# Kernel tuning notes

Hardware: AMD Instinct MI355X
Metric: run time of the kernel (lower is better)

Reference implementation:

```python
import jax, jax.numpy as jnp
import numpy as np

T_STEPS = 64   # number of actions (T-1 in the torch code)
BATCH = 512
STATE = 256
ACTION = 64
BELIEF = 1024
HIDDEN = 1024
EMB = 1024
MIN_STD = 0.1


def setup_inputs() -> dict:
    key = jax.random.key(0)
    ks = jax.random.split(key, 16)
    def w(k, shape):
        return jax.random.normal(k, shape, jnp.float32) * 0.02
    return {
        "s_0": jax.random.normal(ks[0], (BATCH, STATE), jnp.float32),
        "A": jax.random.normal(ks[1], (T_STEPS, BATCH, ACTION), jnp.float32),
        "b_0": jax.random.normal(ks[2], (BATCH, BELIEF), jnp.float32),
        "O": jax.random.normal(ks[3], (T_STEPS, BATCH, EMB), jnp.float32),
        "M": jnp.ones((T_STEPS, BATCH, 1), jnp.float32),
        "noise_pri": jax.random.normal(ks[4], (T_STEPS, BATCH, STATE), jnp.float32),
        "noise_pos": jax.random.normal(ks[5], (T_STEPS, BATCH, STATE), jnp.float32),
        # learned parameters (torch nn.Linear convention: y = x @ W.T + b)
        "W_sa": w(ks[6], (BELIEF, STATE + ACTION)), "b_sa": jnp.zeros((BELIEF,), jnp.float32),
        "W_ih": w(ks[7], (3 * BELIEF, BELIEF)), "b_ih": jnp.zeros((3 * BELIEF,), jnp.float32),
        "W_hh": w(ks[8], (3 * BELIEF, BELIEF)), "b_hh": jnp.zeros((3 * BELIEF,), jnp.float32),
        "W_bpri": w(ks[9], (HIDDEN, BELIEF)), "b_bpri": jnp.zeros((HIDDEN,), jnp.float32),
        "W_spri": w(ks[10], (2 * STATE, HIDDEN)), "b_spri": jnp.zeros((2 * STATE,), jnp.float32),
        "W_bpos": w(ks[11], (HIDDEN, BELIEF + EMB)), "b_bpos": jnp.zeros((HIDDEN,), jnp.float32),
        "W_spos": w(ks[12], (2 * STATE, HIDDEN)), "b_spos": jnp.zeros((2 * STATE,), jnp.float32),
    }


def reference(s_0, A, b_0, O, M, noise_pri, noise_pos,
              W_sa, b_sa, W_ih, b_ih, W_hh, b_hh,
              W_bpri, b_bpri, W_spri, b_spri,
              W_bpos, b_bpos, W_spos, b_spos):
    act = jax.nn.relu  # cfg.activation_function = 'relu'

    def gru_cell(x, h):
        # torch GRUCell gate order: r, z, n
        gi = x @ W_ih.T + b_ih      # [B, 3*BELIEF]
        gh = h @ W_hh.T + b_hh
        i_r, i_z, i_n = jnp.split(gi, 3, axis=1)
        h_r, h_z, h_n = jnp.split(gh, 3, axis=1)
        r = jax.nn.sigmoid(i_r + h_r)
        z = jax.nn.sigmoid(i_z + h_z)
        n = jnp.tanh(i_n + r * h_n)
        return (1.0 - z) * n + z * h

    def step(carry, xs):
        b, s = carry  # belief [B,BELIEF], posterior state [B,STATE]
        a_t, o_t, m_t, eps_p, eps_q = xs
        s_in = s * m_t  # non-terminal mask
        x = act(jnp.concatenate([s_in, a_t], axis=1) @ W_sa.T + b_sa)
        b_new = gru_cell(x, b)
        # prior
        pri = act(b_new @ W_bpri.T + b_bpri) @ W_spri.T + b_spri
        mu_p, hp = jnp.split(pri, 2, axis=1)
        std_p = jax.nn.softplus(hp) + MIN_STD
        s_p = mu_p + std_p * eps_p
        # posterior (uses current observation embedding)
        pos = act(jnp.concatenate([b_new, o_t], axis=1) @ W_bpos.T + b_bpos) @ W_spos.T + b_spos
        mu_q, hq = jnp.split(pos, 2, axis=1)
        std_q = jax.nn.softplus(hq) + MIN_STD
        s_q = mu_q + std_q * eps_q
        return (b_new, s_q), (b_new, s_p, mu_p, std_p, s_q, mu_q, std_q)

    (_, _), ys = jax.lax.scan(step, (b_0, s_0), (A, O, M, noise_pri, noise_pos))
    B_out, S_pri, MU_pri, STD_pri, S_pos, MU_pos, STD_pos = ys
    return B_out, S_pri, MU_pri, STD_pri, S_pos, MU_pos, STD_pos
```

## Files before the change

### kernel.cpp

```cpp
#include <hip/hip_runtime.h>
#include <hip/hip_bf16.h>
#include <math.h>

typedef short bf16x8 __attribute__((ext_vector_type(8)));
typedef float f32x4 __attribute__((ext_vector_type(4)));
typedef unsigned short u16;

#define NT 64
#define NB 512
#define NS 256
#define NA 64
#define NBEL 1024

#define OUT_B      0
#define OUT_SPRI   33554432
#define OUT_MUPRI  41943040
#define OUT_STDPRI 50331648
#define OUT_SPOS   58720256
#define OUT_MUPOS  67108864
#define OUT_STDPOS 75497472

__device__ __forceinline__ f32x4 mfma16(bf16x8 a, bf16x8 b, f32x4 c) {
  return __builtin_amdgcn_mfma_f32_16x16x32_bf16(a, b, c, 0, 0, 0);
}

__device__ __forceinline__ u16 f2bf(float f) {
  union { float f; unsigned u; } v; v.f = f;
  return (u16)((v.u + 0x7FFFu + ((v.u >> 16) & 1u)) >> 16);
}

__device__ __forceinline__ bf16x8 ld8bf(const u16* p) { return *(const bf16x8*)p; }

__device__ __forceinline__ bf16x8 cvt8(const float* p) {
  const float4 lo = *(const float4*)p;
  const float4 hi = *(const float4*)(p + 4);
  bf16x8 v;
  v[0] = (short)f2bf(lo.x); v[1] = (short)f2bf(lo.y);
  v[2] = (short)f2bf(lo.z); v[3] = (short)f2bf(lo.w);
  v[4] = (short)f2bf(hi.x); v[5] = (short)f2bf(hi.y);
  v[6] = (short)f2bf(hi.z); v[7] = (short)f2bf(hi.w);
  return v;
}

__device__ __forceinline__ float sigm(float x) { return 1.f / (1.f + __expf(-x)); }
__device__ __forceinline__ float softplus_(float x) {
  if (x > 20.f) return x;
  return log1pf(__expf(x));
}

#define ZACC(acc) { acc[0][0] = (f32x4){0.f,0.f,0.f,0.f}; acc[0][1] = (f32x4){0.f,0.f,0.f,0.f}; \
                    acc[1][0] = (f32x4){0.f,0.f,0.f,0.f}; acc[1][1] = (f32x4){0.f,0.f,0.f,0.f}; }

#define Q4(acc, a0v, a1v, b0v, b1v) \
  acc[0][0] = mfma16(a0v, b0v, acc[0][0]); \
  acc[0][1] = mfma16(a0v, b1v, acc[0][1]); \
  acc[1][0] = mfma16(a1v, b0v, acc[1][0]); \
  acc[1][1] = mfma16(a1v, b1v, acc[1][1]);

__device__ __forceinline__ void red_write(float* L, f32x4 (&acc)[2][2], int l) {
  const int base = l * 16;
#pragma unroll
  for (int i = 0; i < 2; ++i)
#pragma unroll
    for (int j = 0; j < 2; ++j)
#pragma unroll
      for (int q = 0; q < 4; ++q)
        L[base + (i * 2 + j) * 4 + q] = acc[i][j][q];
}
__device__ __forceinline__ void red_add(const float* L, f32x4 (&acc)[2][2], int l) {
  const int base = l * 16;
#pragma unroll
  for (int i = 0; i < 2; ++i)
#pragma unroll
    for (int j = 0; j < 2; ++j)
#pragma unroll
      for (int q = 0; q < 4; ++q)
        acc[i][j][q] += L[base + (i * 2 + j) * 4 + q];
}

__global__ __launch_bounds__(256) void cvt_weights_k(
    const float* __restrict__ wsa, const float* __restrict__ wih,
    const float* __restrict__ whh, const float* __restrict__ wbpri,
    const float* __restrict__ wspri, const float* __restrict__ wbpos,
    const float* __restrict__ wspos, u16* __restrict__ dst) {
  const int S0 = 327680;
  const int S1 = S0 + 3145728;
  const int S2 = S1 + 3145728;
  const int S3 = S2 + 1048576;
  const int S4 = S3 + 524288;
  const int S5 = S4 + 2097152;
  const int S6 = S5 + 524288;
  for (int i = blockIdx.x * blockDim.x + threadIdx.x; i < S6;
       i += gridDim.x * blockDim.x) {
    float v;
    if (i < S0) v = wsa[i];
    else if (i < S1) v = wih[i - S0];
    else if (i < S2) v = whh[i - S1];
    else if (i < S3) v = wbpri[i - S2];
    else if (i < S4) v = wspri[i - S3];
    else if (i < S5) v = wbpos[i - S4];
    else v = wspos[i - S5];
    dst[i] = f2bf(v);
  }
}

__global__ __launch_bounds__(256) void init_carry_k(
    const float* __restrict__ s0, const float* __restrict__ b0,
    const float* __restrict__ Mptr, u16* __restrict__ smask,
    u16* __restrict__ bbf0, float* __restrict__ hf) {
  for (int i = blockIdx.x * blockDim.x + threadIdx.x; i < NB * NBEL;
       i += gridDim.x * blockDim.x) {
    float b = b0[i];
    bbf0[i] = f2bf(b);
    hf[i] = b;
    if (i < NB * NS) {
      int row = i >> 8;
      smask[i] = f2bf(s0[i] * Mptr[row]);
    }
  }
}

__global__ __launch_bounds__(512, 2) void kA(
    const u16* __restrict__ smask, const float* __restrict__ Af,
    const u16* __restrict__ wsa, const float* __restrict__ bsa,
    u16* __restrict__ xbf, const float* __restrict__ Of,
    const u16* __restrict__ wbpos, float* __restrict__ hbO, int t) {
  __shared__ float lred[4][1024];
  const int l = threadIdx.x & 63, r16 = l & 15, kq = l >> 4;
  const int wid8 = threadIdx.x >> 6;
  const int wid = wid8 & 3, kh = wid8 >> 2;
  if (blockIdx.x < 128) {
    const int g = blockIdx.x, bm = g >> 4, bn = g & 15;
    const int row0 = bm * 64 + (wid >> 1) * 32;
    const int col0 = bn * 64 + (wid & 1) * 32;
    f32x4 acc[2][2]; ZACC(acc);
    const u16* A0 = smask + (row0 + r16) * NS + kq * 8;
    const u16* A1 = A0 + 16 * NS;
    const u16* B0 = wsa + (size_t)(col0 + r16) * 320 + kq * 8;
    const u16* B1 = B0 + 16 * 320;
    if (kh == 0) {
#pragma unroll
      for (int k = 0; k < 160; k += 32) {
        bf16x8 a0 = ld8bf(A0 + k), a1 = ld8bf(A1 + k);
        bf16x8 b0 = ld8bf(B0 + k), b1 = ld8bf(B1 + k);
        Q4(acc, a0, a1, b0, b1);
      }
    } else {
#pragma unroll
      for (int k = 160; k < 256; k += 32) {
        bf16x8 a0 = ld8bf(A0 + k), a1 = ld8bf(A1 + k);
        bf16x8 b0 = ld8bf(B0 + k), b1 = ld8bf(B1 + k);
        Q4(acc, a0, a1, b0, b1);
      }
      const float* F0 = Af + (size_t)t * (NB * NA) + (row0 + r16) * NA + kq * 8;
      const float* F1 = F0 + 16 * NA;
      const u16* C0 = wsa + (size_t)(col0 + r16) * 320 + 256 + kq * 8;
      const u16* C1 = C0 + 16 * 320;
#pragma unroll
      for (int k = 0; k < 64; k += 32) {
        bf16x8 a0 = cvt8(F0 + k), a1 = cvt8(F1 + k);
        bf16x8 b0 = ld8bf(C0 + k), b1 = ld8bf(C1 + k);
        Q4(acc, a0, a1, b0, b1);
      }
      red_write(lred[wid], acc, l);
    }
    __syncthreads();
    if (kh == 0) {
      red_add(lred[wid], acc, l);
#pragma unroll
      for (int i = 0; i < 2; ++i)
#pragma unroll
        for (int j = 0; j < 2; ++j)
#pragma unroll
          for (int q = 0; q < 4; ++q) {
            const int row = row0 + i * 16 + kq * 4 + q;
            const int col = col0 + j * 16 + r16;
            xbf[row * NBEL + col] = f2bf(fmaxf(acc[i][j][q] + bsa[col], 0.f));
          }
    }
  } else {
    const int g = blockIdx.x - 128, bm = g >> 4, bn = g & 15;
    const int row0 = bm * 64 + (wid >> 1) * 32;
    const int col0 = bn * 64 + (wid & 1) * 32;
    f32x4 acc[2][2]; ZACC(acc);
    const float* F0 = Of + (size_t)t * (NB * NBEL) + (row0 + r16) * NBEL + kh * 512 + kq * 8;
    const float* F1 = F0 + 16 * NBEL;
    const u16* B0 = wbpos + (size_t)(col0 + r16) * 2048 + 1024 + kh * 512 + kq * 8;
    const u16* B1 = B0 + 16 * 2048;
#pragma unroll 4
    for (int k = 0; k < 512; k += 32) {
      bf16x8 a0 = cvt8(F0 + k), a1 = cvt8(F1 + k);
      bf16x8 b0 = ld8bf(B0 + k), b1 = ld8bf(B1 + k);
      Q4(acc, a0, a1, b0, b1);
    }
    if (kh == 1) red_write(lred[wid], acc, l);
    __syncthreads();
    if (kh == 0) {
      red_add(lred[wid], acc, l);
#pragma unroll
      for (int i = 0; i < 2; ++i)
#pragma unroll
        for (int j = 0; j < 2; ++j)
#pragma unroll
          for (int q = 0; q < 4; ++q) {
            const int row = row0 + i * 16 + kq * 4 + q;
            const int col = col0 + j * 16 + r16;
            hbO[row * NBEL + col] = acc[i][j][q];
          }
    }
  }
}

__global__ __launch_bounds__(512, 2) void kB(
    const u16* __restrict__ xbf, const u16* __restrict__ bprev,
    const u16* __restrict__ wih, const u16* __restrict__ whh,
    const float* __restrict__ bih, const float* __restrict__ bhh,
    float* __restrict__ hf, u16* __restrict__ bcur, float* __restrict__ out,
    const u16* __restrict__ wbpri, const float* __restrict__ bbpri,
    u16* __restrict__ hpri, int t) {
  __shared__ float lred[4][3][1024];
  const int l = threadIdx.x & 63, r16 = l & 15, kq = l >> 4;
  const int wid8 = threadIdx.x >> 6;
  const int wid = wid8 & 3, kh = wid8 >> 2;
  if (blockIdx.x < 128) {
    if (t >= NT) return;
    const int g = blockIdx.x, bm = g >> 4, bn = g & 15;
    const int row0 = bm * 64 + (wid >> 1) * 32;
    const int col0 = bn * 64 + (wid & 1) * 32;
    f32x4 ar[2][2], az[2][2], an[2][2];
    ZACC(ar); ZACC(az); ZACC(an);
    const u16* Asrc = (kh == 0) ? xbf : bprev;
    const u16* W = (kh == 0) ? wih : whh;
    const u16* A0 = Asrc + (row0 + r16) * NBEL + kq * 8;
    const u16* A1 = A0 + 16 * NBEL;
    const u16* Br0 = W + (size_t)(col0 + r16) * NBEL + kq * 8;
    const u16* Br1 = Br0 + 16 * NBEL;
    const u16* Bz0 = W + (size_t)(col0 + 1024 + r16) * NBEL + kq * 8;
    const u16* Bz1 = Bz0 + 16 * NBEL;
    const u16* Bn0 = W + (size_t)(col0 + 2048 + r16) * NBEL + kq * 8;
    const u16* Bn1 = Bn0 + 16 * NBEL;
#pragma unroll 4
    for (int k = 0; k < NBEL; k += 32) {
      bf16x8 a0 = ld8bf(A0 + k), a1 = ld8bf(A1 + k);
      bf16x8 b0 = ld8bf(Br0 + k), b1 = ld8bf(Br1 + k);
      Q4(ar, a0, a1, b0, b1);
      bf16x8 c0 = ld8bf(Bz0 + k), c1 = ld8bf(Bz1 + k);
      Q4(az, a0, a1, c0, c1);
      bf16x8 d0 = ld8bf(Bn0 + k), d1 = ld8bf(Bn1 + k);
      Q4(an, a0, a1, d0, d1);
    }
    if (kh == 1) {
      red_write(lred[wid][0], ar, l);
      red_write(lred[wid][1], az, l);
      red_write(lred[wid][2], an, l);
    }
    __syncthreads();
    if (kh == 0) {
      const int base = l * 16;
#pragma unroll
      for (int i = 0; i < 2; ++i)
#pragma unroll
        for (int j = 0; j < 2; ++j)
#pragma unroll
          for (int q = 0; q < 4; ++q) {
            const int row = row0 + i * 16 + kq * 4 + q;
            const int c = col0 + j * 16 + r16;
            const int li = base + (i * 2 + j) * 4 + q;
            const float r = sigm(ar[i][j][q] + bih[c] + lred[wid][0][li] + bhh[c]);
            const float z = sigm(az[i][j][q] + bih[c + 1024] + lred[wid][1][li] + bhh[c + 1024]);
            const float n = tanhf(an[i][j][q] + bih[c + 2048] +
                                  r * (lred[wid][2][li] + bhh[c + 2048]));
            const float h = hf[row * NBEL + c];
            const float bnew = (1.f - z) * n + z * h;
            hf[row * NBEL + c] = bnew;
            bcur[row * NBEL + c] = f2bf(bnew);
            out[OUT_B + (size_t)t * (NB * NBEL) + row * NBEL + c] = bnew;
          }
    }
  } else {
    if (t < 1) return;
    const int g = blockIdx.x - 128, bm = g >> 4, bn = g & 15;
    const int row0 = bm * 64 + (wid >> 1) * 32;
    const int col0 = bn * 64 + (wid & 1) * 32;
    f32x4 acc[2][2]; ZACC(acc);
    const u16* A0 = bprev + (row0 + r16) * NBEL + kh * 512 + kq * 8;
    const u16* A1 = A0 + 16 * NBEL;
    const u16* B0 = wbpri + (size_t)(col0 + r16) * NBEL + kh * 512 + kq * 8;
    const u16* B1 = B0 + 16 * NBEL;
#pragma unroll 4
    for (int k = 0; k < 512; k += 32) {
      bf16x8 a0 = ld8bf(A0 + k), a1 = ld8bf(A1 + k);
      bf16x8 b0 = ld8bf(B0 + k), b1 = ld8bf(B1 + k);
      Q4(acc, a0, a1, b0, b1);
    }
    if (kh == 1) red_write(lred[wid][0], acc, l);
    __syncthreads();
    if (kh == 0) {
      red_add(lred[wid][0], acc, l);
#pragma unroll
      for (int i = 0; i < 2; ++i)
#pragma unroll
        for (int j = 0; j < 2; ++j)
#pragma unroll
          for (int q = 0; q < 4; ++q) {
            const int row = row0 + i * 16 + kq * 4 + q;
            const int col = col0 + j * 16 + r16;
            hpri[row * NBEL + col] = f2bf(fmaxf(acc[i][j][q] + bbpri[col], 0.f));
          }
    }
  }
}

__global__ __launch_bounds__(512, 2) void kC(
    const u16* __restrict__ bcur, const u16* __restrict__ wbpos,
    const float* __restrict__ bbpos, const float* __restrict__ hbO,
    u16* __restrict__ hbbf,
    const u16* __restrict__ hpri, const u16* __restrict__ wspri,
    const float* __restrict__ bspri, const float* __restrict__ npri,
    float* __restrict__ out, int t) {
  __shared__ float lred[4][2][1024];
  const int l = threadIdx.x & 63, r16 = l & 15, kq = l >> 4;
  const int wid8 = threadIdx.x >> 6;
  const int wid = wid8 & 3, kh = wid8 >> 2;
  if (blockIdx.x < 128) {
    if (t >= NT) return;
    const int g = blockIdx.x, bm = g >> 4, bn = g & 15;
    const int row0 = bm * 64 + (wid >> 1) * 32;
    const int col0 = bn * 64 + (wid & 1) * 32;
    f32x4 acc[2][2]; ZACC(acc);
    const u16* A0 = bcur + (row0 + r16) * NBEL + kh * 512 + kq * 8;
    const u16* A1 = A0 + 16 * NBEL;
    const u16* B0 = wbpos + (size_t)(col0 + r16) * 2048 + kh * 512 + kq * 8;
    const u16* B1 = B0 + 16 * 2048;
#pragma unroll 4
    for (int k = 0; k < 512; k += 32) {
      bf16x8 a0 = ld8bf(A0 + k), a1 = ld8bf(A1 + k);
      bf16x8 b0 = ld8bf(B0 + k), b1 = ld8bf(B1 + k);
      Q4(acc, a0, a1, b0, b1);
    }
    if (kh == 1) red_write(lred[wid][0], acc, l);
    __syncthreads();
    if (kh == 0) {
      red_add(lred[wid][0], acc, l);
#pragma unroll
      for (int i = 0; i < 2; ++i)
#pragma unroll
        for (int j = 0; j < 2; ++j)
#pragma unroll
          for (int q = 0; q < 4; ++q) {
            const int row = row0 + i * 16 + kq * 4 + q;
            const int col = col0 + j * 16 + r16;
            const float v = acc[i][j][q] + hbO[row * NBEL + col] + bbpos[col];
            hbbf[row * NBEL + col] = f2bf(fmaxf(v, 0.f));
          }
    }
  } else {
    if (t < 1) return;
    const int g = blockIdx.x - 128, bm = g >> 2, bn = g & 3;
    const int row0 = bm * 64 + (wid >> 1) * 32;
    const int c0 = bn * 64 + (wid & 1) * 32;
    f32x4 am[2][2], ah[2][2];
    ZACC(am); ZACC(ah);
    const u16* A0 = hpri + (row0 + r16) * NBEL + kh * 512 + kq * 8;
    const u16* A1 = A0 + 16 * NBEL;
    const u16* Bm0 = wspri + (size_t)(c0 + r16) * NBEL + kh * 512 + kq * 8;
    const u16* Bm1 = Bm0 + 16 * NBEL;
    const u16* Bh0 = wspri + (size_t)(c0 + 256 + r16) * NBEL + kh * 512 + kq * 8;
    const u16* Bh1 = Bh0 + 16 * NBEL;
#pragma unroll 4
    for (int k = 0; k < 512; k += 32) {
      bf16x8 a0 = ld8bf(A0 + k), a1 = ld8bf(A1 + k);
      bf16x8 m0 = ld8bf(Bm0 + k), m1 = ld8bf(Bm1 + k);
      Q4(am, a0, a1, m0, m1);
      bf16x8 h0 = ld8bf(Bh0 + k), h1 = ld8bf(Bh1 + k);
      Q4(ah, a0, a1, h0, h1);
    }
    if (kh == 1) {
      red_write(lred[wid][0], am, l);
      red_write(lred[wid][1], ah, l);
    }
    __syncthreads();
    if (kh == 0) {
      red_add(lred[wid][0], am, l);
      red_add(lred[wid][1], ah, l);
      const int tt = t - 1;
#pragma unroll
      for (int i = 0; i < 2; ++i)
#pragma unroll
        for (int j = 0; j < 2; ++j)
#pragma unroll
          for (int q = 0; q < 4; ++q) {
            const int row = row0 + i * 16 + kq * 4 + q;
            const int c = c0 + j * 16 + r16;
            const size_t idx = (size_t)tt * (NB * NS) + row * NS + c;
            const float mu = am[i][j][q] + bspri[c];
            const float hp = ah[i][j][q] + bspri[c + 256];
            const float sd = softplus_(hp) + 0.1f;
            out[OUT_SPRI + idx] = mu + sd * npri[idx];
            out[OUT_MUPRI + idx] = mu;
            out[OUT_STDPRI + idx] = sd;
          }
    }
  }
}

__global__ __launch_bounds__(512, 2) void kD(
    const u16* __restrict__ hbbf, const u16* __restrict__ wspos,
    const float* __restrict__ bspos, const float* __restrict__ npos,
    const float* __restrict__ Mptr, float* __restrict__ out,
    u16* __restrict__ smask, int t) {
  __shared__ float lred[4][2][1024];
  const int l = threadIdx.x & 63, r16 = l & 15, kq = l >> 4;
  const int wid8 = threadIdx.x >> 6;
  const int wid = wid8 & 3, kh = wid8 >> 2;
  const int g = blockIdx.x, bm = g >> 2, bn = g & 3;
  const int row0 = bm * 64 + (wid >> 1) * 32;
  const int c0 = bn * 64 + (wid & 1) * 32;
  f32x4 am[2][2], ah[2][2];
  ZACC(am); ZACC(ah);
  const u16* A0 = hbbf + (row0 + r16) * NBEL + kh * 512 + kq * 8;
  const u16* A1 = A0 + 16 * NBEL;
  const u16* Bm0 = wspos + (size_t)(c0 + r16) * NBEL + kh * 512 + kq * 8;
  const u16* Bm1 = Bm0 + 16 * NBEL;
  const u16* Bh0 = wspos + (size_t)(c0 + 256 + r16) * NBEL + kh * 512 + kq * 8;
  const u16* Bh1 = Bh0 + 16 * NBEL;
#pragma unroll 4
  for (int k = 0; k < 512; k += 32) {
    bf16x8 a0 = ld8bf(A0 + k), a1 = ld8bf(A1 + k);
    bf16x8 m0 = ld8bf(Bm0 + k), m1 = ld8bf(Bm1 + k);
    Q4(am, a0, a1, m0, m1);
    bf16x8 h0 = ld8bf(Bh0 + k), h1 = ld8bf(Bh1 + k);
    Q4(ah, a0, a1, h0, h1);
  }
  if (kh == 1) {
    red_write(lred[wid][0], am, l);
    red_write(lred[wid][1], ah, l);
  }
  __syncthreads();
  if (kh == 0) {
    red_add(lred[wid][0], am, l);
    red_add(lred[wid][1], ah, l);
#pragma unroll
    for (int i = 0; i < 2; ++i)
#pragma unroll
      for (int j = 0; j < 2; ++j)
#pragma unroll
        for (int q = 0; q < 4; ++q) {
          const int row = row0 + i * 16 + kq * 4 + q;
          const int c = c0 + j * 16 + r16;
          const float mu = am[i][j][q] + bspos[c];
          const float hq = ah[i][j][q] + bspos[c + 256];
          const float sd = softplus_(hq) + 0.1f;
          const size_t idx = (size_t)t * (NB * NS) + row * NS + c;
          const float sq = mu + sd * npos[idx];
          out[OUT_SPOS + idx] = sq;
          out[OUT_MUPOS + idx] = mu;
          out[OUT_STDPOS + idx] = sd;
          const float mn = (t < NT - 1) ? Mptr[(t + 1) * NB + row] : 1.f;
          smask[row * NS + c] = f2bf(sq * mn);
        }
  }
}

extern "C" void kernel_launch(void* const* d_in, const int* in_sizes, int n_in,
                              void* d_out, int out_size, void* d_ws, size_t ws_size,
                              hipStream_t stream) {
  const float* s0 = (const float*)d_in[0];
  const float* Af = (const float*)d_in[1];
  const float* b0 = (const float*)d_in[2];
  const float* Of = (const float*)d_in[3];
  const float* Mp = (const float*)d_in[4];
  const float* npri = (const float*)d_in[5];
  const float* npos = (const float*)d_in[6];
  const float* Wsa = (const float*)d_in[7];
  const float* bsa = (const float*)d_in[8];
  const float* Wih = (const float*)d_in[9];
  const float* bih = (const float*)d_in[10];
  const float* Whh = (const float*)d_in[11];
  const float* bhh = (const float*)d_in[12];
  const float* Wbpri = (const float*)d_in[13];
  const float* bbpri = (const float*)d_in[14];
  const float* Wspri = (const float*)d_in[15];
  const float* bspri = (const float*)d_in[16];
  const float* Wbpos = (const float*)d_in[17];
  const float* bbpos = (const float*)d_in[18];
  const float* Wspos = (const float*)d_in[19];
  const float* bspos = (const float*)d_in[20];

  float* out = (float*)d_out;
  char* ws = (char*)d_ws;
  u16* wbase   = (u16*)ws;
  u16* wsa_b   = wbase;
  u16* wih_b   = wbase + 327680;
  u16* whh_b   = wbase + 3473408;
  u16* wbpri_b = wbase + 6619136;
  u16* wspri_b = wbase + 7667712;
  u16* wbpos_b = wbase + 8192000;
  u16* wspos_b = wbase + 10289152;
  u16*   smask = (u16*)  (ws + 21626880);
  u16*   bbf0  = (u16*)  (ws + 21889024);
  u16*   bbf1  = (u16*)  (ws + 22937600);
  float* hf    = (float*)(ws + 23986176);
  u16*   xbf   = (u16*)  (ws + 26083328);
  float* hbO   = (float*)(ws + 27131904);
  u16*   hbbf  = (u16*)  (ws + 29229056);
  u16*   hpri  = (u16*)  (ws + 30277632);

  cvt_weights_k<<<2048, 256, 0, stream>>>(Wsa, Wih, Whh, Wbpri, Wspri, Wbpos,
                                          Wspos, wbase);
  init_carry_k<<<2048, 256, 0, stream>>>(s0, b0, Mp, smask, bbf0, hf);

  for (int t = 0; t < NT; ++t) {
    const u16* bprev = (t & 1) ? bbf1 : bbf0;
    u16* bcur = (t & 1) ? bbf0 : bbf1;
    kA<<<256, 512, 0, stream>>>(smask, Af, wsa_b, bsa, xbf, Of, wbpos_b, hbO, t);
    kB<<<256, 512, 0, stream>>>(xbf, bprev, wih_b, whh_b, bih, bhh, hf, bcur,
                                out, wbpri_b, bbpri, hpri, t);
    kC<<<160, 512, 0, stream>>>(bcur, wbpos_b, bbpos, hbO, hbbf,
                                hpri, wspri_b, bspri, npri, out, t);
    kD<<<32, 512, 0, stream>>>(hbbf, wspos_b, bspos, npos, Mp, out, smask, t);
  }
  {
    const int t = NT;
    const u16* bprev = (t & 1) ? bbf1 : bbf0;
    u16* bcur = (t & 1) ? bbf0 : bbf1;
    kB<<<256, 512, 0, stream>>>(xbf, bprev, wih_b, whh_b, bih, bhh, hf, bcur,
                                out, wbpri_b, bbpri, hpri, t);
    kC<<<160, 512, 0, stream>>>(bcur, wbpos_b, bbpos, hbO, hbbf,
                                hpri, wspri_b, bspri, npri, out, t);
  }
}
```

Measured before the change: 10.06 ms.

## Restructure recurrent step into three fused kernels with cross-step prefetch

Reorganizes the per-timestep pipeline from four kernels (kA/kB/kC/kD) into three (kL1/kL2/kL3). The observation-embedding GEMM for step t+1 moves into kL2, and the next step's state-action GEMM moves into kL3 after the posterior head. The prior-state head for step t-1 now runs alongside the GRU in kL1, and a prologue kernel computes step 0's inputs. The aim is fewer launches and serial dependencies per step, at the cost of double-buffered hbO, a small 16-block kL3 doing full-K GEMMs serially, and more complex scheduling.

```diff
diff --git a/kernel.cpp b/kernel.cpp
--- a/kernel.cpp
+++ b/kernel.cpp
@@ -120,11 +120,62 @@
   }
 }
 
-__global__ __launch_bounds__(512, 2) void kA(
+__device__ __forceinline__ void dev_spri(
+    int g, int wid, int kh, int r16, int kq, int l, int tt,
+    const u16* __restrict__ hpri, const u16* __restrict__ wspri,
+    const float* __restrict__ bspri, const float* __restrict__ npri,
+    float* __restrict__ out, float* lred0, float* lred1) {
+  const int bm = g >> 2, bn = g & 3;
+  const int row0 = bm * 64 + (wid >> 1) * 32;
+  const int c0 = bn * 64 + (wid & 1) * 32;
+  f32x4 am[2][2], ah[2][2];
+  ZACC(am); ZACC(ah);
+  const u16* A0 = hpri + (row0 + r16) * NBEL + kh * 512 + kq * 8;
+  const u16* A1 = A0 + 16 * NBEL;
+  const u16* Bm0 = wspri + (size_t)(c0 + r16) * NBEL + kh * 512 + kq * 8;
+  const u16* Bm1 = Bm0 + 16 * NBEL;
+  const u16* Bh0 = wspri + (size_t)(c0 + 256 + r16) * NBEL + kh * 512 + kq * 8;
+  const u16* Bh1 = Bh0 + 16 * NBEL;
+#pragma unroll 4
+  for (int k = 0; k < 512; k += 32) {
+    bf16x8 a0 = ld8bf(A0 + k), a1 = ld8bf(A1 + k);
+    bf16x8 m0 = ld8bf(Bm0 + k), m1 = ld8bf(Bm1 + k);
+    Q4(am, a0, a1, m0, m1);
+    bf16x8 h0 = ld8bf(Bh0 + k), h1 = ld8bf(Bh1 + k);
+    Q4(ah, a0, a1, h0, h1);
+  }
+  if (kh == 1) {
+    red_write(lred0, am, l);
+    red_write(lred1, ah, l);
+  }
+  __syncthreads();
+  if (kh == 0) {
+    red_add(lred0, am, l);
+    red_add(lred1, ah, l);
+#pragma unroll
+    for (int i = 0; i < 2; ++i)
+#pragma unroll
+      for (int j = 0; j < 2; ++j)
+#pragma unroll
+        for (int q = 0; q < 4; ++q) {
+          const int row = row0 + i * 16 + kq * 4 + q;
+          const int c = c0 + j * 16 + r16;
+          const size_t idx = (size_t)tt * (NB * NS) + (size_t)row * NS + c;
+          const float mu = am[i][j][q] + bspri[c];
+          const float hp = ah[i][j][q] + bspri[c + 256];
+          const float sd = softplus_(hp) + 0.1f;
+          out[OUT_SPRI + idx] = mu + sd * npri[idx];
+          out[OUT_MUPRI + idx] = mu;
+          out[OUT_STDPRI + idx] = sd;
+        }
+  }
+}
+
+__global__ __launch_bounds__(512, 2) void kX0(
     const u16* __restrict__ smask, const float* __restrict__ Af,
     const u16* __restrict__ wsa, const float* __restrict__ bsa,
-    u16* __restrict__ xbf, const float* __restrict__ Of,
-    const u16* __restrict__ wbpos, float* __restrict__ hbO, int t) {
+    u16* __restrict__ xg, const float* __restrict__ Of,
+    const u16* __restrict__ wbpos, float* __restrict__ hbO0) {
   __shared__ float lred[4][1024];
   const int l = threadIdx.x & 63, r16 = l & 15, kq = l >> 4;
   const int wid8 = threadIdx.x >> 6;
@@ -152,7 +203,7 @@
         bf16x8 b0 = ld8bf(B0 + k), b1 = ld8bf(B1 + k);
         Q4(acc, a0, a1, b0, b1);
       }
-      const float* F0 = Af + (size_t)t * (NB * NA) + (row0 + r16) * NA + kq * 8;
+      const float* F0 = Af + (row0 + r16) * NA + kq * 8;
       const float* F1 = F0 + 16 * NA;
       const u16* C0 = wsa + (size_t)(col0 + r16) * 320 + 256 + kq * 8;
       const u16* C1 = C0 + 16 * 320;
@@ -175,7 +226,7 @@
           for (int q = 0; q < 4; ++q) {
             const int row = row0 + i * 16 + kq * 4 + q;
             const int col = col0 + j * 16 + r16;
-            xbf[row * NBEL + col] = f2bf(fmaxf(acc[i][j][q] + bsa[col], 0.f));
+            xg[row * NBEL + col] = f2bf(fmaxf(acc[i][j][q] + bsa[col], 0.f));
           }
     }
   } else {
@@ -183,7 +234,7 @@
     const int row0 = bm * 64 + (wid >> 1) * 32;
     const int col0 = bn * 64 + (wid & 1) * 32;
     f32x4 acc[2][2]; ZACC(acc);
-    const float* F0 = Of + (size_t)t * (NB * NBEL) + (row0 + r16) * NBEL + kh * 512 + kq * 8;
+    const float* F0 = Of + (row0 + r16) * NBEL + kh * 512 + kq * 8;
     const float* F1 = F0 + 16 * NBEL;
     const u16* B0 = wbpos + (size_t)(col0 + r16) * 2048 + 1024 + kh * 512 + kq * 8;
     const u16* B1 = B0 + 16 * 2048;
@@ -205,31 +256,30 @@
           for (int q = 0; q < 4; ++q) {
             const int row = row0 + i * 16 + kq * 4 + q;
             const int col = col0 + j * 16 + r16;
-            hbO[row * NBEL + col] = acc[i][j][q];
+            hbO0[row * NBEL + col] = acc[i][j][q];
           }
     }
   }
 }
 
-__global__ __launch_bounds__(512, 2) void kB(
-    const u16* __restrict__ xbf, const u16* __restrict__ bprev,
+__global__ __launch_bounds__(512, 2) void kL1(
+    const u16* __restrict__ xg, const u16* __restrict__ bprev,
     const u16* __restrict__ wih, const u16* __restrict__ whh,
     const float* __restrict__ bih, const float* __restrict__ bhh,
     float* __restrict__ hf, u16* __restrict__ bcur, float* __restrict__ out,
-    const u16* __restrict__ wbpri, const float* __restrict__ bbpri,
-    u16* __restrict__ hpri, int t) {
+    const u16* __restrict__ hpri, const u16* __restrict__ wspri,
+    const float* __restrict__ bspri, const float* __restrict__ npri, int t) {
   __shared__ float lred[4][3][1024];
   const int l = threadIdx.x & 63, r16 = l & 15, kq = l >> 4;
   const int wid8 = threadIdx.x >> 6;
   const int wid = wid8 & 3, kh = wid8 >> 2;
   if (blockIdx.x < 128) {
-    if (t >= NT) return;
     const int g = blockIdx.x, bm = g >> 4, bn = g & 15;
     const int row0 = bm * 64 + (wid >> 1) * 32;
     const int col0 = bn * 64 + (wid & 1) * 32;
     f32x4 ar[2][2], az[2][2], an[2][2];
     ZACC(ar); ZACC(az); ZACC(an);
-    const u16* Asrc = (kh == 0) ? xbf : bprev;
+    const u16* Asrc = (kh == 0) ? xg : bprev;
     const u16* W = (kh == 0) ? wih : whh;
     const u16* A0 = Asrc + (row0 + r16) * NBEL + kq * 8;
     const u16* A1 = A0 + 16 * NBEL;
@@ -250,9 +300,9 @@
       Q4(an, a0, a1, d0, d1);
     }
     if (kh == 1) {
-      red_write(lred[wid][0], ar, l);
-      red_write(lred[wid][1], az, l);
-      red_write(lred[wid][2], an, l);
+      red_write(&lred[wid][0][0], ar, l);
+      red_write(&lred[wid][1][0], az, l);
+      red_write(&lred[wid][2][0], an, l);
     }
     __syncthreads();
     if (kh == 0) {
@@ -277,53 +327,25 @@
             out[OUT_B + (size_t)t * (NB * NBEL) + row * NBEL + c] = bnew;
           }
     }
-  } else {
-    if (t < 1) return;
-    const int g = blockIdx.x - 128, bm = g >> 4, bn = g & 15;
-    const int row0 = bm * 64 + (wid >> 1) * 32;
-    const int col0 = bn * 64 + (wid & 1) * 32;
-    f32x4 acc[2][2]; ZACC(acc);
-    const u16* A0 = bprev + (row0 + r16) * NBEL + kh * 512 + kq * 8;
-    const u16* A1 = A0 + 16 * NBEL;
-    const u16* B0 = wbpri + (size_t)(col0 + r16) * NBEL + kh * 512 + kq * 8;
-    const u16* B1 = B0 + 16 * NBEL;
-#pragma unroll 4
-    for (int k = 0; k < 512; k += 32) {
-      bf16x8 a0 = ld8bf(A0 + k), a1 = ld8bf(A1 + k);
-      bf16x8 b0 = ld8bf(B0 + k), b1 = ld8bf(B1 + k);
-      Q4(acc, a0, a1, b0, b1);
-    }
-    if (kh == 1) red_write(lred[wid][0], acc, l);
-    __syncthreads();
-    if (kh == 0) {
-      red_add(lred[wid][0], acc, l);
-#pragma unroll
-      for (int i = 0; i < 2; ++i)
-#pragma unroll
-        for (int j = 0; j < 2; ++j)
-#pragma unroll
-          for (int q = 0; q < 4; ++q) {
-            const int row = row0 + i * 16 + kq * 4 + q;
-            const int col = col0 + j * 16 + r16;
-            hpri[row * NBEL + col] = f2bf(fmaxf(acc[i][j][q] + bbpri[col], 0.f));
-          }
-    }
-  }
-}
-
-__global__ __launch_bounds__(512, 2) void kC(
+  } else if (t >= 1) {
+    dev_spri(blockIdx.x - 128, wid, kh, r16, kq, l, t - 1,
+             hpri, wspri, bspri, npri, out,
+             &lred[wid][0][0], &lred[wid][1][0]);
+  }
+}
+
+__global__ __launch_bounds__(512, 2) void kL2(
     const u16* __restrict__ bcur, const u16* __restrict__ wbpos,
-    const float* __restrict__ bbpos, const float* __restrict__ hbO,
+    const float* __restrict__ bbpos, const float* __restrict__ hbOc,
     u16* __restrict__ hbbf,
-    const u16* __restrict__ hpri, const u16* __restrict__ wspri,
-    const float* __restrict__ bspri, const float* __restrict__ npri,
-    float* __restrict__ out, int t) {
-  __shared__ float lred[4][2][1024];
+    const u16* __restrict__ wbpri, const float* __restrict__ bbpri,
+    u16* __restrict__ hpri,
+    const float* __restrict__ Of, float* __restrict__ hbOn, int t) {
+  __shared__ float lred[4][1024];
   const int l = threadIdx.x & 63, r16 = l & 15, kq = l >> 4;
   const int wid8 = threadIdx.x >> 6;
   const int wid = wid8 & 3, kh = wid8 >> 2;
   if (blockIdx.x < 128) {
-    if (t >= NT) return;
     const int g = blockIdx.x, bm = g >> 4, bn = g & 15;
     const int row0 = bm * 64 + (wid >> 1) * 32;
     const int col0 = bn * 64 + (wid & 1) * 32;
@@ -338,10 +360,10 @@
       bf16x8 b0 = ld8bf(B0 + k), b1 = ld8bf(B1 + k);
       Q4(acc, a0, a1, b0, b1);
     }
-    if (kh == 1) red_write(lred[wid][0], acc, l);
+    if (kh == 1) red_write(lred[wid], acc, l);
     __syncthreads();
     if (kh == 0) {
-      red_add(lred[wid][0], acc, l);
+      red_add(lred[wid], acc, l);
 #pragma unroll
       for (int i = 0; i < 2; ++i)
 #pragma unroll
@@ -350,40 +372,29 @@
           for (int q = 0; q < 4; ++q) {
             const int row = row0 + i * 16 + kq * 4 + q;
             const int col = col0 + j * 16 + r16;
-            const float v = acc[i][j][q] + hbO[row * NBEL + col] + bbpos[col];
+            const float v = acc[i][j][q] + hbOc[row * NBEL + col] + bbpos[col];
             hbbf[row * NBEL + col] = f2bf(fmaxf(v, 0.f));
           }
     }
-  } else {
-    if (t < 1) return;
-    const int g = blockIdx.x - 128, bm = g >> 2, bn = g & 3;
+  } else if (blockIdx.x < 256) {
+    const int g = blockIdx.x - 128, bm = g >> 4, bn = g & 15;
     const int row0 = bm * 64 + (wid >> 1) * 32;
-    const int c0 = bn * 64 + (wid & 1) * 32;
-    f32x4 am[2][2], ah[2][2];
-    ZACC(am); ZACC(ah);
-    const u16* A0 = hpri + (row0 + r16) * NBEL + kh * 512 + kq * 8;
+    const int col0 = bn * 64 + (wid & 1) * 32;
+    f32x4 acc[2][2]; ZACC(acc);
+    const u16* A0 = bcur + (row0 + r16) * NBEL + kh * 512 + kq * 8;
     const u16* A1 = A0 + 16 * NBEL;
-    const u16* Bm0 = wspri + (size_t)(c0 + r16) * NBEL + kh * 512 + kq * 8;
-    const u16* Bm1 = Bm0 + 16 * NBEL;
-    const u16* Bh0 = wspri + (size_t)(c0 + 256 + r16) * NBEL + kh * 512 + kq * 8;
-    const u16* Bh1 = Bh0 + 16 * NBEL;
+    const u16* B0 = wbpri + (size_t)(col0 + r16) * NBEL + kh * 512 + kq * 8;
+    const u16* B1 = B0 + 16 * NBEL;
 #pragma unroll 4
     for (int k = 0; k < 512; k += 32) {
       bf16x8 a0 = ld8bf(A0 + k), a1 = ld8bf(A1 + k);
-      bf16x8 m0 = ld8bf(Bm0 + k), m1 = ld8bf(Bm1 + k);
-      Q4(am, a0, a1, m0, m1);
-      bf16x8 h0 = ld8bf(Bh0 + k), h1 = ld8bf(Bh1 + k);
-      Q4(ah, a0, a1, h0, h1);
-    }
-    if (kh == 1) {
-      red_write(lred[wid][0], am, l);
-      red_write(lred[wid][1], ah, l);
-    }
+      bf16x8 b0 = ld8bf(B0 + k), b1 = ld8bf(B1 + k);
+      Q4(acc, a0, a1, b0, b1);
+    }
+    if (kh == 1) red_write(lred[wid], acc, l);
     __syncthreads();
     if (kh == 0) {
-      red_add(lred[wid][0], am, l);
-      red_add(lred[wid][1], ah, l);
-      const int tt = t - 1;
+      red_add(lred[wid], acc, l);
 #pragma unroll
       for (int i = 0; i < 2; ++i)
 #pragma unroll
@@ -391,74 +402,146 @@
 #pragma unroll
           for (int q = 0; q < 4; ++q) {
             const int row = row0 + i * 16 + kq * 4 + q;
-            const int c = c0 + j * 16 + r16;
-            const size_t idx = (size_t)tt * (NB * NS) + row * NS + c;
-            const float mu = am[i][j][q] + bspri[c];
-            const float hp = ah[i][j][q] + bspri[c + 256];
-            const float sd = softplus_(hp) + 0.1f;
-            out[OUT_SPRI + idx] = mu + sd * npri[idx];
-            out[OUT_MUPRI + idx] = mu;
-            out[OUT_STDPRI + idx] = sd;
+            const int col = col0 + j * 16 + r16;
+            hpri[row * NBEL + col] = f2bf(fmaxf(acc[i][j][q] + bbpri[col], 0.f));
           }
     }
-  }
-}
-
-__global__ __launch_bounds__(512, 2) void kD(
+  } else {
+    if (t + 1 >= NT) return;
+    const int g = blockIdx.x - 256, bm = g >> 4, bn = g & 15;
+    const int row0 = bm * 64 + (wid >> 1) * 32;
+    const int col0 = bn * 64 + (wid & 1) * 32;
+    f32x4 acc[2][2]; ZACC(acc);
+    const float* F0 = Of + (size_t)(t + 1) * (NB * NBEL) + (row0 + r16) * NBEL + kh * 512 + kq * 8;
+    const float* F1 = F0 + 16 * NBEL;
+    const u16* B0 = wbpos + (size_t)(col0 + r16) * 2048 + 1024 + kh * 512 + kq * 8;
+    const u16* B1 = B0 + 16 * 2048;
+#pragma unroll 4
+    for (int k = 0; k < 512; k += 32) {
+      bf16x8 a0 = cvt8(F0 + k), a1 = cvt8(F1 + k);
+      bf16x8 b0 = ld8bf(B0 + k), b1 = ld8bf(B1 + k);
+      Q4(acc, a0, a1, b0, b1);
+    }
+    if (kh == 1) red_write(lred[wid], acc, l);
+    __syncthreads();
+    if (kh == 0) {
+      red_add(lred[wid], acc, l);
+#pragma unroll
+      for (int i = 0; i < 2; ++i)
+#pragma unroll
+        for (int j = 0; j < 2; ++j)
+#pragma unroll
+          for (int q = 0; q < 4; ++q) {
+            const int row = row0 + i * 16 + kq * 4 + q;
+            const int col = col0 + j * 16 + r16;
+            hbOn[row * NBEL + col] = acc[i][j][q];
+          }
+    }
+  }
+}
+
+__global__ __launch_bounds__(512, 1) void kL3(
     const u16* __restrict__ hbbf, const u16* __restrict__ wspos,
     const float* __restrict__ bspos, const float* __restrict__ npos,
     const float* __restrict__ Mptr, float* __restrict__ out,
-    u16* __restrict__ smask, int t) {
-  __shared__ float lred[4][2][1024];
+    const float* __restrict__ Af, const u16* __restrict__ wsa,
+    const float* __restrict__ bsa, u16* __restrict__ xg,
+    const u16* __restrict__ hpri, const u16* __restrict__ wspri,
+    const float* __restrict__ bspri, const float* __restrict__ npri, int t) {
   const int l = threadIdx.x & 63, r16 = l & 15, kq = l >> 4;
   const int wid8 = threadIdx.x >> 6;
-  const int wid = wid8 & 3, kh = wid8 >> 2;
-  const int g = blockIdx.x, bm = g >> 2, bn = g & 3;
-  const int row0 = bm * 64 + (wid >> 1) * 32;
-  const int c0 = bn * 64 + (wid & 1) * 32;
-  f32x4 am[2][2], ah[2][2];
-  ZACC(am); ZACC(ah);
-  const u16* A0 = hbbf + (row0 + r16) * NBEL + kh * 512 + kq * 8;
-  const u16* A1 = A0 + 16 * NBEL;
-  const u16* Bm0 = wspos + (size_t)(c0 + r16) * NBEL + kh * 512 + kq * 8;
-  const u16* Bm1 = Bm0 + 16 * NBEL;
-  const u16* Bh0 = wspos + (size_t)(c0 + 256 + r16) * NBEL + kh * 512 + kq * 8;
-  const u16* Bh1 = Bh0 + 16 * NBEL;
-#pragma unroll 4
-  for (int k = 0; k < 512; k += 32) {
-    bf16x8 a0 = ld8bf(A0 + k), a1 = ld8bf(A1 + k);
-    bf16x8 m0 = ld8bf(Bm0 + k), m1 = ld8bf(Bm1 + k);
-    Q4(am, a0, a1, m0, m1);
-    bf16x8 h0 = ld8bf(Bh0 + k), h1 = ld8bf(Bh1 + k);
-    Q4(ah, a0, a1, h0, h1);
-  }
-  if (kh == 1) {
-    red_write(lred[wid][0], am, l);
-    red_write(lred[wid][1], ah, l);
+  if (blockIdx.x >= 16) {
+    if (t == NT - 1) {
+      __shared__ float lredS[4][2][1024];
+      const int wid = wid8 & 3, kh = wid8 >> 2;
+      dev_spri(blockIdx.x - 16, wid, kh, r16, kq, l, NT - 1,
+               hpri, wspri, bspri, npri, out,
+               &lredS[wid][0][0], &lredS[wid][1][0]);
+    }
+    return;
+  }
+  __shared__ float stg[2][32][260];
+  __shared__ u16 sm[32][264];
+  const int rb = blockIdx.x * 32;
+  const int gem = wid8 >> 2, ct = wid8 & 3;
+#pragma unroll
+  for (int jt = 0; jt < 2; ++jt) {
+    const int c0 = ct * 64 + jt * 32;
+    f32x4 acc[2][2]; ZACC(acc);
+    const u16* A0 = hbbf + (size_t)(rb + r16) * NBEL + kq * 8;
+    const u16* A1 = A0 + 16 * NBEL;
+    const u16* B0 = wspos + (size_t)(gem * 256 + c0 + r16) * NBEL + kq * 8;
+    const u16* B1 = B0 + 16 * NBEL;
+#pragma unroll 4
+    for (int k = 0; k < NBEL; k += 32) {
+      bf16x8 a0 = ld8bf(A0 + k), a1 = ld8bf(A1 + k);
+      bf16x8 b0 = ld8bf(B0 + k), b1 = ld8bf(B1 + k);
+      Q4(acc, a0, a1, b0, b1);
+    }
+#pragma unroll
+    for (int i = 0; i < 2; ++i)
+#pragma unroll
+      for (int j = 0; j < 2; ++j)
+#pragma unroll
+        for (int q = 0; q < 4; ++q)
+          stg[gem][i * 16 + kq * 4 + q][c0 + j * 16 + r16] = acc[i][j][q];
   }
   __syncthreads();
-  if (kh == 0) {
-    red_add(lred[wid][0], am, l);
-    red_add(lred[wid][1], ah, l);
-#pragma unroll
-    for (int i = 0; i < 2; ++i)
-#pragma unroll
-      for (int j = 0; j < 2; ++j)
-#pragma unroll
-        for (int q = 0; q < 4; ++q) {
-          const int row = row0 + i * 16 + kq * 4 + q;
-          const int c = c0 + j * 16 + r16;
-          const float mu = am[i][j][q] + bspos[c];
-          const float hq = ah[i][j][q] + bspos[c + 256];
-          const float sd = softplus_(hq) + 0.1f;
-          const size_t idx = (size_t)t * (NB * NS) + row * NS + c;
-          const float sq = mu + sd * npos[idx];
-          out[OUT_SPOS + idx] = sq;
-          out[OUT_MUPOS + idx] = mu;
-          out[OUT_STDPOS + idx] = sd;
-          const float mn = (t < NT - 1) ? Mptr[(t + 1) * NB + row] : 1.f;
-          smask[row * NS + c] = f2bf(sq * mn);
-        }
+  {
+    const int rr = threadIdx.x >> 4;
+    const int cb = (threadIdx.x & 15) * 16;
+    const int row = rb + rr;
+    const float mn = (t < NT - 1) ? Mptr[(t + 1) * NB + row] : 1.f;
+#pragma unroll 4
+    for (int e = 0; e < 16; ++e) {
+      const int c = cb + e;
+      const float mu = stg[0][rr][c] + bspos[c];
+      const float hq = stg[1][rr][c] + bspos[c + 256];
+      const float sd = softplus_(hq) + 0.1f;
+      const size_t idx = (size_t)t * (NB * NS) + (size_t)row * NS + c;
+      const float sq = mu + sd * npos[idx];
+      out[OUT_SPOS + idx] = sq;
+      out[OUT_MUPOS + idx] = mu;
+      out[OUT_STDPOS + idx] = sd;
+      sm[rr][c] = f2bf(sq * mn);
+    }
+  }
+  __syncthreads();
+  if (t + 1 < NT) {
+#pragma unroll
+    for (int jt = 0; jt < 4; ++jt) {
+      const int c0 = wid8 * 128 + jt * 32;
+      f32x4 acc[2][2]; ZACC(acc);
+      const u16* B0 = wsa + (size_t)(c0 + r16) * 320 + kq * 8;
+      const u16* B1 = B0 + 16 * 320;
+#pragma unroll
+      for (int k = 0; k < 256; k += 32) {
+        bf16x8 a0 = *(const bf16x8*)&sm[r16][k + kq * 8];
+        bf16x8 a1 = *(const bf16x8*)&sm[16 + r16][k + kq * 8];
+        bf16x8 b0 = ld8bf(B0 + k), b1 = ld8bf(B1 + k);
+        Q4(acc, a0, a1, b0, b1);
+      }
+      const float* F0 = Af + (size_t)(t + 1) * (NB * NA) + (size_t)(rb + r16) * NA + kq * 8;
+      const float* F1 = F0 + 16 * NA;
+      const u16* C0 = wsa + (size_t)(c0 + r16) * 320 + 256 + kq * 8;
+      const u16* C1 = C0 + 16 * 320;
+#pragma unroll
+      for (int k = 0; k < 64; k += 32) {
+        bf16x8 a0 = cvt8(F0 + k), a1 = cvt8(F1 + k);
+        bf16x8 b0 = ld8bf(C0 + k), b1 = ld8bf(C1 + k);
+        Q4(acc, a0, a1, b0, b1);
+      }
+#pragma unroll
+      for (int i = 0; i < 2; ++i)
+#pragma unroll
+        for (int j = 0; j < 2; ++j)
+#pragma unroll
+          for (int q = 0; q < 4; ++q) {
+            const int row = rb + i * 16 + kq * 4 + q;
+            const int col = c0 + j * 16 + r16;
+            xg[row * NBEL + col] = f2bf(fmaxf(acc[i][j][q] + bsa[col], 0.f));
+          }
+    }
   }
 }
 
@@ -501,32 +584,28 @@
   u16*   bbf0  = (u16*)  (ws + 21889024);
   u16*   bbf1  = (u16*)  (ws + 22937600);
   float* hf    = (float*)(ws + 23986176);
-  u16*   xbf   = (u16*)  (ws + 26083328);
-  float* hbO   = (float*)(ws + 27131904);
-  u16*   hbbf  = (u16*)  (ws + 29229056);
-  u16*   hpri  = (u16*)  (ws + 30277632);
+  u16*   xg    = (u16*)  (ws + 26083328);
+  float* hbO0  = (float*)(ws + 27131904);
+  float* hbO1  = (float*)(ws + 29229056);
+  u16*   hbbf  = (u16*)  (ws + 31326208);
+  u16*   hpri  = (u16*)  (ws + 32374784);
 
   cvt_weights_k<<<2048, 256, 0, stream>>>(Wsa, Wih, Whh, Wbpri, Wspri, Wbpos,
                                           Wspos, wbase);
   init_carry_k<<<2048, 256, 0, stream>>>(s0, b0, Mp, smask, bbf0, hf);
+  kX0<<<256, 512, 0, stream>>>(smask, Af, wsa_b, bsa, xg, Of, wbpos_b, hbO0);
 
   for (int t = 0; t < NT; ++t) {
     const u16* bprev = (t & 1) ? bbf1 : bbf0;
     u16* bcur = (t & 1) ? bbf0 : bbf1;
-    kA<<<256, 512, 0, stream>>>(smask, Af, wsa_b, bsa, xbf, Of, wbpos_b, hbO, t);
-    kB<<<256, 512, 0, stream>>>(xbf, bprev, wih_b, whh_b, bih, bhh, hf, bcur,
-                                out, wbpri_b, bbpri, hpri, t);
-    kC<<<160, 512, 0, stream>>>(bcur, wbpos_b, bbpos, hbO, hbbf,
-                                hpri, wspri_b, bspri, npri, out, t);
-    kD<<<32, 512, 0, stream>>>(hbbf, wspos_b, bspos, npos, Mp, out, smask, t);
-  }
-  {
-    const int t = NT;
-    const u16* bprev = (t & 1) ? bbf1 : bbf0;
-    u16* bcur = (t & 1) ? bbf0 : bbf1;
-    kB<<<256, 512, 0, stream>>>(xbf, bprev, wih_b, whh_b, bih, bhh, hf, bcur,
-                                out, wbpri_b, bbpri, hpri, t);
-    kC<<<160, 512, 0, stream>>>(bcur, wbpos_b, bbpos, hbO, hbbf,
-                                hpri, wspri_b, bspri, npri, out, t);
-  }
-}
+    float* hbOc = (t & 1) ? hbO1 : hbO0;
+    float* hbOn = (t & 1) ? hbO0 : hbO1;
+    kL1<<<160, 512, 0, stream>>>(xg, bprev, wih_b, whh_b, bih, bhh, hf, bcur,
+                                 out, hpri, wspri_b, bspri, npri, t);
+    kL2<<<384, 512, 0, stream>>>(bcur, wbpos_b, bbpos, hbOc, hbbf,
+                                 wbpri_b, bbpri, hpri, Of, hbOn, t);
+    kL3<<<48, 512, 0, stream>>>(hbbf, wspos_b, bspos, npos, Mp, out,
+                                Af, wsa_b, bsa, xg,
+                                hpri, wspri_b, bspri, npri, t);
+  }
+}
```

New measurement: 13.54 ms. 34.6% more time.
